# Performance work log

Hardware: AMD Instinct MI355X
Metric: run time of the kernel (lower is better)

## Reference

```python
import jax, jax.numpy as jnp
import numpy as np


def _cdist(x, y):
    # x: (b, n, c), y: (b, m, c) -> (b, n, m) Euclidean distances
    x2 = jnp.sum(x * x, axis=-1, keepdims=True)          # (b, n, 1)
    y2 = jnp.sum(y * y, axis=-1)[:, None, :]             # (b, 1, m)
    xy = jnp.einsum('bnc,bmc->bnm', x, y)                # (b, n, m)
    d2 = jnp.maximum(x2 + y2 - 2.0 * xy, 0.0)
    return jnp.sqrt(d2)


def setup_inputs() -> dict:
    key = jax.random.key(0)
    k1, k2, k3, k4 = jax.random.split(key, 4)
    bs, N, M, C = 8, 4096, 4096, 128
    return {
        'set1': jax.random.normal(k1, (bs, N, C), dtype=jnp.float32),
        'set2': jax.random.normal(k2, (bs, M, C), dtype=jnp.float32),
        'w1': jax.random.uniform(k3, (bs, N), dtype=jnp.float32),
        'w2': jax.random.uniform(k4, (bs, M), dtype=jnp.float32),
    }


def reference(set1, set2, w1, w2):
    dist = _cdist(set1, set2)                 # (b, N, M)
    out_dist = jnp.min(dist, axis=2)          # (b, N)
    out_dist2 = jnp.min(dist, axis=1)         # (b, M)
    total = (jnp.sum(w1 * out_dist) + jnp.sum(w2 * out_dist2)) / 2.0
    return total
```

## Files before the change

### kernel.cpp

```cpp
#include <hip/hip_runtime.h>

#define BS 8
#define NN 4096
#define MM 4096
#define CC 128
#define XT 128
#define MT 128
#define MH 2048
#define NMT (MH / MT)
#define NXT (NN / XT)

#define FINF_BITS 0x7F800000u

typedef __attribute__((ext_vector_type(8))) short bf16x8;
typedef __attribute__((ext_vector_type(4))) float f32x4;

__device__ inline ushort f2bf(float f) {
    unsigned u = __float_as_uint(f);
    unsigned r = (u + 0x7FFFu + ((u >> 16) & 1u)) >> 16;
    return (ushort)r;
}

__global__ void ch_prep(const float* __restrict__ y,
                        ushort* __restrict__ y16, float* __restrict__ yn,
                        unsigned* __restrict__ rowmin, unsigned* __restrict__ colmin,
                        float* __restrict__ out) {
    int gid = blockIdx.x * blockDim.x + threadIdx.x;
    size_t i = (size_t)gid * 4;

    float4 w = *(const float4*)(y + i);
    ushort4 p;
    p.x = f2bf(w.x); p.y = f2bf(w.y); p.z = f2bf(w.z); p.w = f2bf(w.w);
    *(ushort4*)(y16 + i) = p;
    float sy = w.x * w.x + w.y * w.y + w.z * w.z + w.w * w.w;

#pragma unroll
    for (int mask = 1; mask <= 16; mask <<= 1)
        sy += __shfl_xor(sy, mask, 64);
    if ((threadIdx.x & 31) == 0)
        yn[gid >> 5] = sy;

    if (gid < BS * NN) rowmin[gid] = FINF_BITS;
    if (gid < BS * MM) colmin[gid] = FINF_BITS;
    if (gid == 0) out[0] = 0.0f;
}

__global__ __launch_bounds__(512) void ch_tile(
    const float* __restrict__ Xf, const ushort* __restrict__ Y,
    const float* __restrict__ yn,
    unsigned* __restrict__ rowmin, unsigned* __restrict__ colmin) {

    __shared__ ushort xs[XT * CC];
    __shared__ unsigned coltile[MH];
    __shared__ unsigned rowtile[XT];
    __shared__ float xnorm[XT];

    const int b  = blockIdx.x;
    const int xt = blockIdx.y;
    const int mh = blockIdx.z;
    const int n0 = xt * XT;
    const int m0 = mh * MH;
    const int tid  = threadIdx.x;
    const int wave = tid >> 6;
    const int lane = tid & 63;
    const int lc   = lane & 15;
    const int quad = lane >> 4;
    const int wm = wave >> 2;
    const int wn = wave & 3;

    const float* Xb = Xf + ((size_t)b * NN + n0) * CC;
    {
        float psum[4];
#pragma unroll
        for (int s = 0; s < 4; ++s) {
            int flat = s * 512 + tid;
            int r = flat >> 4, c = flat & 15;
            float4 v0 = *(const float4*)(Xb + (size_t)r * CC + c * 8);
            float4 v1 = *(const float4*)(Xb + (size_t)r * CC + c * 8 + 4);
            ushort h[8] = {f2bf(v0.x), f2bf(v0.y), f2bf(v0.z), f2bf(v0.w),
                           f2bf(v1.x), f2bf(v1.y), f2bf(v1.z), f2bf(v1.w)};
            *(bf16x8*)(xs + r * CC + (c ^ (r & 7)) * 8) = *(bf16x8*)h;
            psum[s] = v0.x * v0.x + v0.y * v0.y + v0.z * v0.z + v0.w * v0.w +
                      v1.x * v1.x + v1.y * v1.y + v1.z * v1.z + v1.w * v1.w;
        }
#pragma unroll
        for (int mask = 1; mask <= 8; mask <<= 1)
#pragma unroll
            for (int s = 0; s < 4; ++s)
                psum[s] += __shfl_xor(psum[s], mask, 64);
        if ((tid & 15) == 0) {
#pragma unroll
            for (int s = 0; s < 4; ++s)
                xnorm[s * 32 + (tid >> 4)] = psum[s];
        }
    }
    for (int c2 = tid; c2 < MH; c2 += 512) coltile[c2] = FINF_BITS;
    if (tid < XT) rowtile[tid] = FINF_BITS;
    __syncthreads();

    float xnp[4][4];
#pragma unroll
    for (int i = 0; i < 4; ++i) {
        float4 t = *(const float4*)(&xnorm[wm * 64 + i * 16 + quad * 4]);
        xnp[i][0] = t.x; xnp[i][1] = t.y; xnp[i][2] = t.z; xnp[i][3] = t.w;
    }
    float rm[4][4];
#pragma unroll
    for (int i = 0; i < 4; ++i)
#pragma unroll
        for (int r = 0; r < 4; ++r) rm[i][r] = __builtin_inff();

    const ushort* Yb  = Y + ((size_t)b * MM + m0) * CC;
    const float*  ynb = yn + (size_t)b * MM + m0;
    const int xrow = (wm * 64 + lc) * CC;
    const int xsw  = lc & 7;

#pragma unroll 1
    for (int mt = 0; mt < NMT; ++mt) {
        const ushort* Ymt = Yb + (size_t)(mt * MT + wn * 32 + lc) * CC + quad * 8;

        float ynr[2];
#pragma unroll
        for (int j = 0; j < 2; ++j)
            ynr[j] = ynb[mt * MT + wn * 32 + j * 16 + lc];

        f32x4 acc[4][2];
        const f32x4 z = {0.f, 0.f, 0.f, 0.f};
#pragma unroll
        for (int kt = 0; kt < 4; ++kt) {
            bf16x8 af[4], yf[2];
            const int cs = ((kt * 4 + quad) ^ xsw) * 8;
#pragma unroll
            for (int j = 0; j < 2; ++j)
                yf[j] = *(const bf16x8*)(Ymt + (size_t)j * 16 * CC + kt * 32);
#pragma unroll
            for (int i = 0; i < 4; ++i)
                af[i] = *(const bf16x8*)(xs + xrow + i * 16 * CC + cs);
#pragma unroll
            for (int j = 0; j < 2; ++j)
#pragma unroll
                for (int i = 0; i < 4; ++i)
                    acc[i][j] = __builtin_amdgcn_mfma_f32_16x16x32_bf16(
                        af[i], yf[j], (kt == 0) ? z : acc[i][j], 0, 0, 0);
        }

        float cmv[2];
#pragma unroll
        for (int j = 0; j < 2; ++j) cmv[j] = __builtin_inff();

#pragma unroll
        for (int i = 0; i < 4; ++i) {
#pragma unroll
            for (int j = 0; j < 2; ++j) {
                f32x4 a = acc[i][j];
#pragma unroll
                for (int r = 0; r < 4; ++r) {
                    float d2 = xnp[i][r] + fmaf(-2.0f, a[r], ynr[j]);
                    rm[i][r] = fminf(rm[i][r], d2);
                    cmv[j]   = fminf(cmv[j], d2);
                }
            }
        }

#pragma unroll
        for (int mask = 16; mask <= 32; mask <<= 1)
#pragma unroll
            for (int j = 0; j < 2; ++j)
                cmv[j] = fminf(cmv[j], __shfl_xor(cmv[j], mask, 64));
        if (quad == 0) {
#pragma unroll
            for (int j = 0; j < 2; ++j)
                atomicMin(&coltile[mt * MT + wn * 32 + j * 16 + lc],
                          __float_as_uint(fmaxf(cmv[j], 0.0f)));
        }
    }

#pragma unroll
    for (int mask = 1; mask <= 8; mask <<= 1)
#pragma unroll
        for (int i = 0; i < 4; ++i)
#pragma unroll
            for (int r = 0; r < 4; ++r)
                rm[i][r] = fminf(rm[i][r], __shfl_xor(rm[i][r], mask, 64));
    if (lc == 0) {
#pragma unroll
        for (int i = 0; i < 4; ++i)
#pragma unroll
            for (int r = 0; r < 4; ++r)
                atomicMin(&rowtile[wm * 64 + i * 16 + quad * 4 + r],
                          __float_as_uint(fmaxf(rm[i][r], 0.0f)));
    }

    __syncthreads();
    if (tid < XT)
        atomicMin(&rowmin[(size_t)b * NN + n0 + tid], rowtile[tid]);
    for (int c2 = tid; c2 < MH; c2 += 512)
        atomicMin(&colmin[(size_t)b * MM + m0 + c2], coltile[c2]);
}

__global__ void ch_finalize(const unsigned* __restrict__ rowmin,
                            const unsigned* __restrict__ colmin,
                            const float* __restrict__ w1,
                            const float* __restrict__ w2,
                            float* __restrict__ out) {
    int i = blockIdx.x * blockDim.x + threadIdx.x;
    int stride = gridDim.x * blockDim.x;
    float s = 0.f;
    for (int idx = i; idx < BS * NN; idx += stride)
        s += w1[idx] * sqrtf(__uint_as_float(rowmin[idx])) +
             w2[idx] * sqrtf(__uint_as_float(colmin[idx]));
#pragma unroll
    for (int off = 32; off > 0; off >>= 1) s += __shfl_down(s, off, 64);
    __shared__ float ls[4];
    int lane = threadIdx.x & 63, wv = threadIdx.x >> 6;
    if (lane == 0) ls[wv] = s;
    __syncthreads();
    if (threadIdx.x == 0) {
        float t = ls[0] + ls[1] + ls[2] + ls[3];
        atomicAdd(out, 0.5f * t);
    }
}

extern "C" void kernel_launch(void* const* d_in, const int* in_sizes, int n_in,
                              void* d_out, int out_size, void* d_ws, size_t ws_size,
                              hipStream_t stream) {
    const float* set1 = (const float*)d_in[0];
    const float* set2 = (const float*)d_in[1];
    const float* w1   = (const float*)d_in[2];
    const float* w2   = (const float*)d_in[3];
    float* out = (float*)d_out;

    ushort*   y16    = (ushort*)d_ws;
    float*    yn     = (float*)(y16 + (size_t)BS * MM * CC);
    unsigned* rowmin = (unsigned*)(yn + BS * MM);
    unsigned* colmin = rowmin + BS * NN;

    ch_prep<<<BS * MM * CC / 4 / 256, 256, 0, stream>>>(
        set2, y16, yn, rowmin, colmin, out);

    dim3 grid(BS, NXT, MM / MH);
    ch_tile<<<grid, 512, 0, stream>>>(set1, y16, yn, rowmin, colmin);

    ch_finalize<<<64, 256, 0, stream>>>(rowmin, colmin, w1, w2, out);
}
```

Measured before the change: 150.5 us.

## Stage Y tiles in double-buffered LDS via async global_load_lds with 256-thread blocks

Y fragments were previously read straight from global memory by every wave. They are now copied into a double-buffered, XOR-swizzled shared-memory tile with async global-to-LDS loads, prefetching the next 64-row tile while the current one is computed. The block shrinks to 4 waves arranged 2x2, so each Y tile is shared across waves, which cuts redundant global traffic. In exchange it adds a barrier per tile and uses more LDS, which may lower occupancy, and fewer waves are left to hide latency.

After: 130.9 us. 1.15x faster.

```diff
diff --git a/kernel.cpp b/kernel.cpp
--- a/kernel.cpp
+++ b/kernel.cpp
@@ -5,9 +5,9 @@
 #define MM 4096
 #define CC 128
 #define XT 128
-#define MT 128
+#define YT 64
 #define MH 2048
-#define NMT (MH / MT)
+#define NYT (MH / YT)
 #define NXT (NN / XT)
 
 #define FINF_BITS 0x7F800000u
@@ -45,12 +45,13 @@
     if (gid == 0) out[0] = 0.0f;
 }
 
-__global__ __launch_bounds__(512) void ch_tile(
+__global__ __launch_bounds__(256) void ch_tile(
     const float* __restrict__ Xf, const ushort* __restrict__ Y,
     const float* __restrict__ yn,
     unsigned* __restrict__ rowmin, unsigned* __restrict__ colmin) {
 
     __shared__ ushort xs[XT * CC];
+    __shared__ ushort ys[2][YT * CC];
     __shared__ unsigned coltile[MH];
     __shared__ unsigned rowtile[XT];
     __shared__ float xnorm[XT];
@@ -65,15 +66,17 @@
     const int lane = tid & 63;
     const int lc   = lane & 15;
     const int quad = lane >> 4;
-    const int wm = wave >> 2;
-    const int wn = wave & 3;
+    const int wm = wave >> 1;
+    const int wn = wave & 1;
+
+    const ushort* Yb = Y + ((size_t)b * MM + m0) * CC;
 
     const float* Xb = Xf + ((size_t)b * NN + n0) * CC;
     {
-        float psum[4];
-#pragma unroll
-        for (int s = 0; s < 4; ++s) {
-            int flat = s * 512 + tid;
+        float psum[8];
+#pragma unroll
+        for (int s = 0; s < 8; ++s) {
+            int flat = s * 256 + tid;
             int r = flat >> 4, c = flat & 15;
             float4 v0 = *(const float4*)(Xb + (size_t)r * CC + c * 8);
             float4 v1 = *(const float4*)(Xb + (size_t)r * CC + c * 8 + 4);
@@ -86,16 +89,28 @@
 #pragma unroll
         for (int mask = 1; mask <= 8; mask <<= 1)
 #pragma unroll
-            for (int s = 0; s < 4; ++s)
+            for (int s = 0; s < 8; ++s)
                 psum[s] += __shfl_xor(psum[s], mask, 64);
         if ((tid & 15) == 0) {
 #pragma unroll
-            for (int s = 0; s < 4; ++s)
-                xnorm[s * 32 + (tid >> 4)] = psum[s];
-        }
-    }
-    for (int c2 = tid; c2 < MH; c2 += 512) coltile[c2] = FINF_BITS;
+            for (int s = 0; s < 8; ++s)
+                xnorm[s * 16 + (tid >> 4)] = psum[s];
+        }
+    }
+    for (int c2 = tid; c2 < MH; c2 += 256) coltile[c2] = FINF_BITS;
     if (tid < XT) rowtile[tid] = FINF_BITS;
+
+#pragma unroll
+    for (int s = 0; s < 4; ++s) {
+        int f = s * 256 + tid;
+        int r = f >> 4, c = f & 15;
+        const ushort* g = Yb + (size_t)r * CC + (c ^ (r & 15)) * 8;
+        ushort* l = ys[0] + (s * 256 + wave * 64) * 8;
+        __builtin_amdgcn_global_load_lds(
+            (const __attribute__((address_space(1))) void*)g,
+            (__attribute__((address_space(3))) void*)l, 16, 0, 0);
+    }
+
     __syncthreads();
 
     float xnp[4][4];
@@ -110,32 +125,50 @@
 #pragma unroll
         for (int r = 0; r < 4; ++r) rm[i][r] = __builtin_inff();
 
-    const ushort* Yb  = Y + ((size_t)b * MM + m0) * CC;
-    const float*  ynb = yn + (size_t)b * MM + m0;
+    const float* ynb = yn + (size_t)b * MM + m0;
     const int xrow = (wm * 64 + lc) * CC;
+    const int yrow = (wn * 32 + lc) * CC;
     const int xsw  = lc & 7;
 
 #pragma unroll 1
-    for (int mt = 0; mt < NMT; ++mt) {
-        const ushort* Ymt = Yb + (size_t)(mt * MT + wn * 32 + lc) * CC + quad * 8;
+    for (int mt = 0; mt < NYT; ++mt) {
+        if (mt) __syncthreads();
+
+        if (mt + 1 < NYT) {
+            const ushort* Ysrc = Yb + (size_t)(mt + 1) * YT * CC;
+            ushort* dstb = ys[(mt + 1) & 1];
+#pragma unroll
+            for (int s = 0; s < 4; ++s) {
+                int f = s * 256 + tid;
+                int r = f >> 4, c = f & 15;
+                const ushort* g = Ysrc + (size_t)r * CC + (c ^ (r & 15)) * 8;
+                ushort* l = dstb + (s * 256 + wave * 64) * 8;
+                __builtin_amdgcn_global_load_lds(
+                    (const __attribute__((address_space(1))) void*)g,
+                    (__attribute__((address_space(3))) void*)l, 16, 0, 0);
+            }
+        }
+
+        const ushort* yl = ys[mt & 1];
 
         float ynr[2];
 #pragma unroll
         for (int j = 0; j < 2; ++j)
-            ynr[j] = ynb[mt * MT + wn * 32 + j * 16 + lc];
+            ynr[j] = ynb[mt * YT + wn * 32 + j * 16 + lc];
 
         f32x4 acc[4][2];
         const f32x4 z = {0.f, 0.f, 0.f, 0.f};
 #pragma unroll
         for (int kt = 0; kt < 4; ++kt) {
             bf16x8 af[4], yf[2];
-            const int cs = ((kt * 4 + quad) ^ xsw) * 8;
-#pragma unroll
-            for (int j = 0; j < 2; ++j)
-                yf[j] = *(const bf16x8*)(Ymt + (size_t)j * 16 * CC + kt * 32);
+            const int cx = ((kt * 4 + quad) ^ xsw) * 8;
+            const int cy = ((kt * 4 + quad) ^ lc) * 8;
+#pragma unroll
+            for (int j = 0; j < 2; ++j)
+                yf[j] = *(const bf16x8*)(yl + yrow + j * 16 * CC + cy);
 #pragma unroll
             for (int i = 0; i < 4; ++i)
-                af[i] = *(const bf16x8*)(xs + xrow + i * 16 * CC + cs);
+                af[i] = *(const bf16x8*)(xs + xrow + i * 16 * CC + cx);
 #pragma unroll
             for (int j = 0; j < 2; ++j)
 #pragma unroll
@@ -170,7 +203,7 @@
         if (quad == 0) {
 #pragma unroll
             for (int j = 0; j < 2; ++j)
-                atomicMin(&coltile[mt * MT + wn * 32 + j * 16 + lc],
+                atomicMin(&coltile[mt * YT + wn * 32 + j * 16 + lc],
                           __float_as_uint(fmaxf(cmv[j], 0.0f)));
         }
     }
@@ -194,7 +227,7 @@
     __syncthreads();
     if (tid < XT)
         atomicMin(&rowmin[(size_t)b * NN + n0 + tid], rowtile[tid]);
-    for (int c2 = tid; c2 < MH; c2 += 512)
+    for (int c2 = tid; c2 < MH; c2 += 256)
         atomicMin(&colmin[(size_t)b * MM + m0 + c2], coltile[c2]);
 }
 
@@ -239,7 +272,7 @@
         set2, y16, yn, rowmin, colmin, out);
 
     dim3 grid(BS, NXT, MM / MH);
-    ch_tile<<<grid, 512, 0, stream>>>(set1, y16, yn, rowmin, colmin);
+    ch_tile<<<grid, 256, 0, stream>>>(set1, y16, yn, rowmin, colmin);
 
     ch_finalize<<<64, 256, 0, stream>>>(rowmin, colmin, w1, w2, out);
 }
```
